# Optimization experiments

Hardware: AMD Instinct MI355X
Metric: run time of the kernel (lower is better)

## Reference

```python
import jax, jax.numpy as jnp
import numpy as np


def setup_inputs() -> dict:
    key = jax.random.key(0)
    k1, k2, k3, k4 = jax.random.split(key, 4)
    B, Nq, Nc, D = 4, 1024, 16384, 1024
    return {
        "query_embeddings": jax.random.normal(k1, (B, Nq, D), dtype=jnp.float32),
        "context_embeddings": jax.random.normal(k2, (B, Nc, D), dtype=jnp.float32),
        "W": jax.random.normal(k3, (D, D), dtype=jnp.float32) * (1.0 / np.sqrt(D)),
        "b": jax.random.normal(k4, (D,), dtype=jnp.float32) * 0.02,
    }


TOP_N = 5


def _pairwise_l2(q, c):
    # q: [B, Nq, D], c: [B, Nc, D] -> [B, Nq, Nc] Euclidean distances
    q_sq = jnp.sum(q * q, axis=-1, keepdims=True)          # [B, Nq, 1]
    c_sq = jnp.sum(c * c, axis=-1)[:, None, :]             # [B, 1, Nc]
    cross = jnp.einsum("bqd,bcd->bqc", q, c)               # [B, Nq, Nc]
    d2 = jnp.maximum(q_sq + c_sq - 2.0 * cross, 0.0)
    return jnp.sqrt(d2)


def reference(query_embeddings, context_embeddings, W, b):
    # latent query projection (nn.Linear): x @ W.T + b
    q_proj = jnp.einsum("bqd,ed->bqe", query_embeddings, W) + b
    distances = _pairwise_l2(q_proj, context_embeddings)    # [B, Nq, Nc]
    # smallest top_n distances -> top_k on negated values
    neg_d, idx = jax.lax.top_k(-distances, TOP_N)
    return (-neg_d, idx)
```

## Files before the change

### kernel.cpp

```cpp
#include <hip/hip_runtime.h>
#include <cfloat>
#include <math.h>

#define D_DIM 1024
#define B_DIM 4
#define NQ    1024
#define NC    16384
#define TOPN  5
#define TOPA  5
#define CSPLIT 8
#define CAND  (TOPA*CSPLIT)
#define QT    64
#define CTILE 256
#define BK    64

#define PBM 128
#define PBN 64
#define PBK 16
#define PPAD 4

typedef __bf16 bf16x8 __attribute__((ext_vector_type(8)));
typedef float  f32x4  __attribute__((ext_vector_type(4)));
typedef double f64x4  __attribute__((ext_vector_type(4)));

__device__ __forceinline__ unsigned short f2bf(float f) {
    unsigned u = __builtin_bit_cast(unsigned, f);
    unsigned r = (u + 0x7fffu + ((u >> 16) & 1u)) >> 16;
    return (unsigned short)r;
}

__device__ __forceinline__ void gload16(const void* g, void* l) {
    __builtin_amdgcn_global_load_lds(
        (const __attribute__((address_space(1))) unsigned*)g,
        (__attribute__((address_space(3))) unsigned*)l, 16, 0, 0);
}

template<int N, typename T>
__device__ __forceinline__ void topk_insert(T (&bv)[N], int (&bi)[N], T v, int ci) {
    if (v < bv[N-1] || (v == bv[N-1] && ci < bi[N-1])) {
        bv[N-1] = v; bi[N-1] = ci;
        #pragma unroll
        for (int s = N-1; s > 0; --s) {
            bool sw = (bv[s] < bv[s-1]) || (bv[s] == bv[s-1] && bi[s] < bi[s-1]);
            if (sw) {
                T tv = bv[s-1]; bv[s-1] = bv[s]; bv[s] = tv;
                int ti = bi[s-1]; bi[s-1] = bi[s]; bi[s] = ti;
            }
        }
    }
}

template<int N>
__device__ __forceinline__ void insN(float (&bv)[N], int (&bi)[N], float v, int ci) {
    if (v < bv[N-1]) {
        bv[N-1] = v; bi[N-1] = ci;
        #pragma unroll
        for (int s = N-1; s > 0; --s) {
            if (bv[s] < bv[s-1]) {
                float tv = bv[s-1]; bv[s-1] = bv[s]; bv[s] = tv;
                int   ti = bi[s-1]; bi[s-1] = bi[s]; bi[s] = ti;
            }
        }
    }
}

__device__ __forceinline__ void ins5b(float (&bv)[TOPA], int (&bi)[TOPA], float v, int ci) {
    #pragma unroll
    for (int s = 0; s < TOPA; ++s) {
        const bool  c    = v < bv[s];
        const float vmin = c ? v : bv[s];
        const float vmax = c ? bv[s] : v;
        const int   imin = c ? ci : bi[s];
        const int   imax = c ? bi[s] : ci;
        bv[s] = vmin; bi[s] = imin;
        v = vmax; ci = imax;
    }
}

__global__ __launch_bounds__(256) void proj64_mfma_kernel(const float* __restrict__ Q,
                                                          const float* __restrict__ W,
                                                          const float* __restrict__ bias,
                                                          double* __restrict__ P64)
{
    __shared__ float Qs[PBM][PBK + PPAD];
    __shared__ float Ws[PBN][PBK + PPAD];

    const int t    = threadIdx.x;
    const int lane = t & 63;
    const int w    = t >> 6;
    const int l15  = lane & 15;
    const int l4   = lane >> 4;
    const int m0   = blockIdx.y * PBM;
    const int n0   = blockIdx.x * PBN;
    const int wm   = (w >> 1) * 64;
    const int wn   = (w & 1) * 32;

    const int srow = t >> 2;
    const int scol = (t & 3) * 4;

    f64x4 acc[4][2];
    #pragma unroll
    for (int fm = 0; fm < 4; ++fm)
        #pragma unroll
        for (int fn = 0; fn < 2; ++fn) acc[fm][fn] = (f64x4)0.0;

    for (int k0 = 0; k0 < D_DIM; k0 += PBK) {
        float4 qa0 = *(const float4*)&Q[(size_t)(m0 + srow)      * D_DIM + k0 + scol];
        float4 qa1 = *(const float4*)&Q[(size_t)(m0 + srow + 64) * D_DIM + k0 + scol];
        float4 wa  = *(const float4*)&W[(size_t)(n0 + srow)      * D_DIM + k0 + scol];
        __syncthreads();
        *(float4*)&Qs[srow][scol]      = qa0;
        *(float4*)&Qs[srow + 64][scol] = qa1;
        *(float4*)&Ws[srow][scol]      = wa;
        __syncthreads();

        #pragma unroll
        for (int ks = 0; ks < 4; ++ks) {
            const int kc = ks * 4 + l4;
            double a[4], b[2];
            #pragma unroll
            for (int fm = 0; fm < 4; ++fm) a[fm] = (double)Qs[wm + fm * 16 + l15][kc];
            #pragma unroll
            for (int fn = 0; fn < 2; ++fn) b[fn] = (double)Ws[wn + fn * 16 + l15][kc];
            #pragma unroll
            for (int fm = 0; fm < 4; ++fm)
                #pragma unroll
                for (int fn = 0; fn < 2; ++fn)
                    acc[fm][fn] = __builtin_amdgcn_mfma_f64_16x16x4f64(a[fm], b[fn], acc[fm][fn], 0, 0, 0);
        }
    }

    #pragma unroll
    for (int fm = 0; fm < 4; ++fm) {
        #pragma unroll
        for (int fn = 0; fn < 2; ++fn) {
            const int col = n0 + wn + fn * 16 + l15;
            const double bv = (double)bias[col];
            #pragma unroll
            for (int j = 0; j < 4; ++j) {
                const int row = m0 + wm + fm * 16 + j * 4 + l4;
                P64[(size_t)row * D_DIM + col] = acc[fm][fn][j] + bv;
            }
        }
    }
}

__global__ __launch_bounds__(256) void perm_detect_kernel(const float* __restrict__ Q,
                                                          const float* __restrict__ W,
                                                          const float* __restrict__ bias,
                                                          const double* __restrict__ P64,
                                                          int* __restrict__ invperm)
{
    __shared__ double tv[16];
    const int t = threadIdx.x;
    const int g = t >> 4;
    const int s = t & 15;
    if (t < 16) invperm[t] = t;

    double acc = 0.0;
    const int kb = s * 64;
    for (int k = 0; k < 64; ++k)
        acc = fma((double)Q[(size_t)g * D_DIM + kb + k], (double)W[kb + k], acc);
    #pragma unroll
    for (int off = 8; off; off >>= 1) acc += __shfl_down(acc, off, 16);
    if (s == 0) tv[g] = acc + (double)bias[0];
    __syncthreads();

    if (t < 16) {
        double p = P64[(size_t)t * D_DIM];
        int best = 0; double bd = fabs(p - tv[0]);
        #pragma unroll
        for (int i = 1; i < 16; ++i) {
            double d = fabs(p - tv[i]);
            if (d < bd) { bd = d; best = i; }
        }
        invperm[best] = t;
    }
}

__global__ __launch_bounds__(256) void pack_c_kernel(const float* __restrict__ C,
                                                     unsigned short* __restrict__ Cbf,
                                                     float* __restrict__ csq)
{
    int wave = threadIdx.x >> 6;
    int lane = threadIdx.x & 63;
    int row  = blockIdx.x * 4 + wave;
    const float* x = C + (size_t)row * D_DIM;
    float s = 0.f;
    #pragma unroll
    for (int i = 0; i < 4; ++i) {
        float4 v = *(const float4*)&x[lane * 4 + i * 256];
        s += v.x * v.x + v.y * v.y + v.z * v.z + v.w * v.w;
        ushort4 h;
        h.x = f2bf(v.x); h.y = f2bf(v.y); h.z = f2bf(v.z); h.w = f2bf(v.w);
        *(ushort4*)&Cbf[(size_t)row * D_DIM + lane * 4 + i * 256] = h;
    }
    #pragma unroll
    for (int off = 32; off; off >>= 1) s += __shfl_down(s, off, 64);
    if (lane == 0) csq[row] = s;
}

__global__ __launch_bounds__(256) void pack_q_kernel(const double* __restrict__ P64,
                                                     const int* __restrict__ invperm,
                                                     unsigned short* __restrict__ Pbf,
                                                     float* __restrict__ qsq)
{
    int wave = threadIdx.x >> 6;
    int lane = threadIdx.x & 63;
    int row  = blockIdx.x * 4 + wave;
    int prow = (row & ~15) | invperm[row & 15];
    const double* x = P64 + (size_t)prow * D_DIM;
    float s = 0.f;
    #pragma unroll
    for (int j = 0; j < 8; ++j) {
        double2 v = *(const double2*)&x[lane * 2 + j * 128];
        float a = (float)v.x, b = (float)v.y;
        s += a * a + b * b;
        ushort2 h; h.x = f2bf(a); h.y = f2bf(b);
        *(ushort2*)&Pbf[(size_t)row * D_DIM + lane * 2 + j * 128] = h;
    }
    #pragma unroll
    for (int off = 32; off; off >>= 1) s += __shfl_down(s, off, 64);
    if (lane == 0) qsq[row] = s;
}

__global__ __launch_bounds__(256, 3) void dist_mfma_kernel(const unsigned short* __restrict__ Pbf,
                                                           const unsigned short* __restrict__ Cbf,
                                                           const float* __restrict__ qsq,
                                                           const float* __restrict__ csq,
                                                           int* __restrict__ pi)
{
    __shared__ __align__(16) short CsS[CTILE * 64];
    __shared__ __align__(16) short QsS[QT * 64];
    float* MV = (float*)CsS;
    int*   MI = (int*)(CsS + 4096);

    const int t    = threadIdx.x;
    const int lane = t & 63;
    const int w    = t >> 6;
    const int l15  = lane & 15;
    const int l4   = lane >> 4;
    const int r8   = lane >> 3;
    const int sc   = lane & 7;
    const int csplit = blockIdx.x;
    const int by = blockIdx.y;
    const int bz = blockIdx.z;
    const int qg0 = bz * NQ + by * QT;

    unsigned cOff[8], qOff[2];
    #pragma unroll
    for (int j = 0; j < 8; ++j)
        cOff[j] = (unsigned)((w * 64 + j * 8 + r8) * D_DIM + (sc ^ r8) * 8);
    #pragma unroll
    for (int j = 0; j < 2; ++j)
        qOff[j] = (unsigned)((w * 16 + j * 8 + r8) * D_DIM + (sc ^ r8) * 8);

    float qsv[4];
    #pragma unroll
    for (int s = 0; s < 4; ++s) qsv[s] = qsq[qg0 + s * 16 + l15];

    float bv[4][TOPA]; int bi[4][TOPA];
    #pragma unroll
    for (int s = 0; s < 4; ++s)
        #pragma unroll
        for (int j = 0; j < TOPA; ++j) { bv[s][j] = FLT_MAX; bi[s][j] = 0x7fffffff; }

    const int cpb = NC / CSPLIT;
    for (int it = 0; it < cpb / CTILE; ++it) {
        const int cg0 = csplit * cpb + it * CTILE;
        const size_t crow0 = (size_t)bz * NC + cg0;

        f32x4 acc[4][4];
        #pragma unroll
        for (int u = 0; u < 4; ++u)
            #pragma unroll
            for (int s = 0; s < 4; ++s) acc[u][s] = (f32x4)0.0f;

        for (int k0 = 0; k0 < D_DIM; k0 += BK) {
            const unsigned short* cB = Cbf + crow0 * D_DIM + k0;
            const unsigned short* qB = Pbf + (size_t)qg0 * D_DIM + k0;
            __syncthreads();
            #pragma unroll
            for (int j = 0; j < 8; ++j)
                gload16(cB + cOff[j], &CsS[(w * 64 + j * 8) * 64]);
            #pragma unroll
            for (int j = 0; j < 2; ++j)
                gload16(qB + qOff[j], &QsS[(w * 16 + j * 8) * 64]);
            __syncthreads();
            #pragma unroll
            for (int ks = 0; ks < 2; ++ks) {
                const int sp = ((ks * 4 + l4) ^ (l15 & 7)) * 8;
                bf16x8 bq[4], ac[4];
                #pragma unroll
                for (int s = 0; s < 4; ++s)
                    bq[s] = *(const bf16x8*)&QsS[(s * 16 + l15) * 64 + sp];
                #pragma unroll
                for (int u = 0; u < 4; ++u)
                    ac[u] = *(const bf16x8*)&CsS[(w * 64 + u * 16 + l15) * 64 + sp];
                #pragma unroll
                for (int u = 0; u < 4; ++u)
                    #pragma unroll
                    for (int s = 0; s < 4; ++s)
                        acc[u][s] = __builtin_amdgcn_mfma_f32_16x16x32_bf16(ac[u], bq[s], acc[u][s], 0, 0, 0);
            }
        }

        #pragma unroll
        for (int u = 0; u < 4; ++u) {
            const int crow = w * 64 + u * 16 + l4 * 4;
            float4 cs4 = *(const float4*)&csq[(size_t)bz * NC + cg0 + crow];
            float csa[4] = {cs4.x, cs4.y, cs4.z, cs4.w};
            #pragma unroll
            for (int s = 0; s < 4; ++s) {
                #pragma unroll
                for (int r = 0; r < 4; ++r) {
                    float v = qsv[s] + csa[r] - 2.0f * acc[u][s][r];
                    ins5b(bv[s], bi[s], v, cg0 + crow + r);
                }
            }
        }
    }

    #pragma unroll
    for (int mask = 16; mask <= 32; mask <<= 1) {
        #pragma unroll
        for (int s = 0; s < 4; ++s) {
            float ov[TOPA]; int oi[TOPA];
            #pragma unroll
            for (int j = 0; j < TOPA; ++j) {
                ov[j] = __shfl_xor(bv[s][j], mask, 64);
                oi[j] = __shfl_xor(bi[s][j], mask, 64);
            }
            #pragma unroll
            for (int j = 0; j < TOPA; ++j) insN<TOPA>(bv[s], bi[s], ov[j], oi[j]);
        }
    }
    __syncthreads();
    if (l4 == 0) {
        #pragma unroll
        for (int s = 0; s < 4; ++s) {
            int q = s * 16 + l15;
            #pragma unroll
            for (int j = 0; j < TOPA; ++j) {
                MV[(q * 4 + w) * TOPA + j] = bv[s][j];
                MI[(q * 4 + w) * TOPA + j] = bi[s][j];
            }
        }
    }
    __syncthreads();
    if (t < QT) {
        float mv[TOPA]; int mi[TOPA];
        #pragma unroll
        for (int j = 0; j < TOPA; ++j) { mv[j] = FLT_MAX; mi[j] = 0x7fffffff; }
        for (int l = 0; l < 4; ++l)
            #pragma unroll
            for (int j = 0; j < TOPA; ++j)
                insN<TOPA>(mv, mi, MV[(t * 4 + l) * TOPA + j], MI[(t * 4 + l) * TOPA + j]);
        size_t base = (((size_t)qg0 + t) * CSPLIT + csplit) * TOPA;
        #pragma unroll
        for (int j = 0; j < TOPA; ++j) pi[base + j] = mi[j];
    }
}

__global__ __launch_bounds__(256) void refine_kernel(const double* __restrict__ P64,
                                                     const int* __restrict__ invperm,
                                                     const float* __restrict__ C,
                                                     const int*   __restrict__ pi,
                                                     float* __restrict__ out)
{
    __shared__ double dvs[CAND];
    __shared__ int    dis[CAND];
    const int q    = blockIdx.x;
    const int pq   = (q & ~15) | invperm[q & 15];
    const int bz   = q >> 10;
    const int t    = threadIdx.x;
    const int wave = t >> 6;
    const int lane = t & 63;
    const double* p = P64 + (size_t)pq * D_DIM;

    for (int k = wave; k < CAND; k += 4) {
        int ci = pi[(size_t)q * CAND + k];
        const float* c = C + ((size_t)bz * NC + ci) * D_DIM;
        double s = 0.0;
        #pragma unroll
        for (int j = 0; j < 16; ++j) {
            int d = lane + 64 * j;
            double diff = p[d] - (double)c[d];
            s = fma(diff, diff, s);
        }
        #pragma unroll
        for (int off = 32; off; off >>= 1) s += __shfl_down(s, off, 64);
        if (lane == 0) { dvs[k] = s; dis[k] = ci; }
    }
    __syncthreads();
    if (t == 0) {
        double bv[TOPN]; int bi[TOPN];
        #pragma unroll
        for (int j = 0; j < TOPN; ++j) { bv[j] = DBL_MAX; bi[j] = 0x7fffffff; }
        for (int k = 0; k < CAND; ++k)
            topk_insert<TOPN,double>(bv, bi, dvs[k], dis[k]);
        #pragma unroll
        for (int j = 0; j < TOPN; ++j) {
            out[(size_t)q * TOPN + j] = (float)sqrt(bv[j]);
            out[(size_t)B_DIM * NQ * TOPN + (size_t)q * TOPN + j] = (float)bi[j];
        }
    }
}

extern "C" void kernel_launch(void* const* d_in, const int* in_sizes, int n_in,
                              void* d_out, int out_size, void* d_ws, size_t ws_size,
                              hipStream_t stream) {
    const float* Q    = (const float*)d_in[0];
    const float* C    = (const float*)d_in[1];
    const float* W    = (const float*)d_in[2];
    const float* bias = (const float*)d_in[3];
    float* out = (float*)d_out;

    char* ws = (char*)d_ws;
    double*         P64 = (double*)ws;
    unsigned short* Pbf = (unsigned short*)(ws + (size_t)32 * 1024 * 1024);
    unsigned short* Cbf = (unsigned short*)(ws + (size_t)40 * 1024 * 1024);
    float*          qsq = (float*)(ws + (size_t)168 * 1024 * 1024);
    float*          csq = qsq + 4096;
    int*            pi  = (int*)(csq + 65536);
    int*            ivp = pi + (size_t)B_DIM * NQ * CAND;

    proj64_mfma_kernel<<<dim3(D_DIM / PBN, (B_DIM * NQ) / PBM), 256, 0, stream>>>(Q, W, bias, P64);
    perm_detect_kernel<<<1, 256, 0, stream>>>(Q, W, bias, P64, ivp);
    pack_c_kernel<<<(B_DIM * NC) / 4, 256, 0, stream>>>(C, Cbf, csq);
    pack_q_kernel<<<(B_DIM * NQ) / 4, 256, 0, stream>>>(P64, ivp, Pbf, qsq);
    dist_mfma_kernel<<<dim3(CSPLIT, NQ / QT, B_DIM), 256, 0, stream>>>(Pbf, Cbf, qsq, csq, pi);
    refine_kernel<<<B_DIM * NQ, 256, 0, stream>>>(P64, ivp, C, pi, out);
}
```

Measured before the change: 925.6 us.

## Double query tile with 8-wave dist blocks and fuse C packing into projection

The distance kernel now uses 512-thread blocks covering 128 queries. Waves are split into two query halves by four candidate quarters, so each C tile loaded into LDS is reused across twice as many queries, halving C traffic per query. Separately, the C bf16 packing blocks are appended to the projection kernel's grid, which removes one launch and lets the memory-bound packing overlap with the compute-bound projection. Costs include higher LDS use, occupancy limited to 2 blocks per CU, and half as many distance blocks.

```diff
diff --git a/kernel.cpp b/kernel.cpp
--- a/kernel.cpp
+++ b/kernel.cpp
@@ -10,7 +10,7 @@
 #define TOPA  5
 #define CSPLIT 8
 #define CAND  (TOPA*CSPLIT)
-#define QT    64
+#define QT    128
 #define CTILE 256
 #define BK    64
 
@@ -18,6 +18,7 @@
 #define PBN 64
 #define PBK 16
 #define PPAD 4
+#define PROJ_BLKS ((D_DIM/PBN) * ((B_DIM*NQ)/PBM))
 
 typedef __bf16 bf16x8 __attribute__((ext_vector_type(8)));
 typedef float  f32x4  __attribute__((ext_vector_type(4)));
@@ -77,11 +78,34 @@
     }
 }
 
-__global__ __launch_bounds__(256) void proj64_mfma_kernel(const float* __restrict__ Q,
-                                                          const float* __restrict__ W,
-                                                          const float* __restrict__ bias,
-                                                          double* __restrict__ P64)
+__global__ __launch_bounds__(256) void proj_packc_kernel(const float* __restrict__ Q,
+                                                         const float* __restrict__ W,
+                                                         const float* __restrict__ bias,
+                                                         const float* __restrict__ C,
+                                                         double* __restrict__ P64,
+                                                         unsigned short* __restrict__ Cbf,
+                                                         float* __restrict__ csq)
 {
+    const int bid = blockIdx.x;
+    if (bid >= PROJ_BLKS) {
+        int wave = threadIdx.x >> 6;
+        int lane = threadIdx.x & 63;
+        int row  = (bid - PROJ_BLKS) * 4 + wave;
+        const float* x = C + (size_t)row * D_DIM;
+        float s = 0.f;
+        #pragma unroll
+        for (int i = 0; i < 4; ++i) {
+            float4 v = *(const float4*)&x[lane * 4 + i * 256];
+            s += v.x * v.x + v.y * v.y + v.z * v.z + v.w * v.w;
+            ushort4 h;
+            h.x = f2bf(v.x); h.y = f2bf(v.y); h.z = f2bf(v.z); h.w = f2bf(v.w);
+            *(ushort4*)&Cbf[(size_t)row * D_DIM + lane * 4 + i * 256] = h;
+        }
+        #pragma unroll
+        for (int off = 32; off; off >>= 1) s += __shfl_down(s, off, 64);
+        if (lane == 0) csq[row] = s;
+        return;
+    }
     __shared__ float Qs[PBM][PBK + PPAD];
     __shared__ float Ws[PBN][PBK + PPAD];
 
@@ -90,8 +114,8 @@
     const int w    = t >> 6;
     const int l15  = lane & 15;
     const int l4   = lane >> 4;
-    const int m0   = blockIdx.y * PBM;
-    const int n0   = blockIdx.x * PBN;
+    const int m0   = (bid >> 4) * PBM;
+    const int n0   = (bid & 15) * PBN;
     const int wm   = (w >> 1) * 64;
     const int wn   = (w & 1) * 32;
 
@@ -178,28 +202,6 @@
     }
 }
 
-__global__ __launch_bounds__(256) void pack_c_kernel(const float* __restrict__ C,
-                                                     unsigned short* __restrict__ Cbf,
-                                                     float* __restrict__ csq)
-{
-    int wave = threadIdx.x >> 6;
-    int lane = threadIdx.x & 63;
-    int row  = blockIdx.x * 4 + wave;
-    const float* x = C + (size_t)row * D_DIM;
-    float s = 0.f;
-    #pragma unroll
-    for (int i = 0; i < 4; ++i) {
-        float4 v = *(const float4*)&x[lane * 4 + i * 256];
-        s += v.x * v.x + v.y * v.y + v.z * v.z + v.w * v.w;
-        ushort4 h;
-        h.x = f2bf(v.x); h.y = f2bf(v.y); h.z = f2bf(v.z); h.w = f2bf(v.w);
-        *(ushort4*)&Cbf[(size_t)row * D_DIM + lane * 4 + i * 256] = h;
-    }
-    #pragma unroll
-    for (int off = 32; off; off >>= 1) s += __shfl_down(s, off, 64);
-    if (lane == 0) csq[row] = s;
-}
-
 __global__ __launch_bounds__(256) void pack_q_kernel(const double* __restrict__ P64,
                                                      const int* __restrict__ invperm,
                                                      unsigned short* __restrict__ Pbf,
@@ -224,7 +226,7 @@
     if (lane == 0) qsq[row] = s;
 }
 
-__global__ __launch_bounds__(256, 3) void dist_mfma_kernel(const unsigned short* __restrict__ Pbf,
+__global__ __launch_bounds__(512, 2) void dist_mfma_kernel(const unsigned short* __restrict__ Pbf,
                                                            const unsigned short* __restrict__ Cbf,
                                                            const float* __restrict__ qsq,
                                                            const float* __restrict__ csq,
@@ -233,11 +235,13 @@
     __shared__ __align__(16) short CsS[CTILE * 64];
     __shared__ __align__(16) short QsS[QT * 64];
     float* MV = (float*)CsS;
-    int*   MI = (int*)(CsS + 4096);
+    int*   MI = (int*)(CsS + 5120);
 
     const int t    = threadIdx.x;
     const int lane = t & 63;
     const int w    = t >> 6;
+    const int wq   = w >> 2;
+    const int wc   = w & 3;
     const int l15  = lane & 15;
     const int l4   = lane >> 4;
     const int r8   = lane >> 3;
@@ -247,17 +251,17 @@
     const int bz = blockIdx.z;
     const int qg0 = bz * NQ + by * QT;
 
-    unsigned cOff[8], qOff[2];
-    #pragma unroll
-    for (int j = 0; j < 8; ++j)
-        cOff[j] = (unsigned)((w * 64 + j * 8 + r8) * D_DIM + (sc ^ r8) * 8);
+    unsigned cOff[4], qOff[2];
+    #pragma unroll
+    for (int j = 0; j < 4; ++j)
+        cOff[j] = (unsigned)((wc * 64 + wq * 32 + j * 8 + r8) * D_DIM + (sc ^ r8) * 8);
     #pragma unroll
     for (int j = 0; j < 2; ++j)
         qOff[j] = (unsigned)((w * 16 + j * 8 + r8) * D_DIM + (sc ^ r8) * 8);
 
     float qsv[4];
     #pragma unroll
-    for (int s = 0; s < 4; ++s) qsv[s] = qsq[qg0 + s * 16 + l15];
+    for (int s = 0; s < 4; ++s) qsv[s] = qsq[qg0 + wq * 64 + s * 16 + l15];
 
     float bv[4][TOPA]; int bi[4][TOPA];
     #pragma unroll
@@ -281,8 +285,8 @@
             const unsigned short* qB = Pbf + (size_t)qg0 * D_DIM + k0;
             __syncthreads();
             #pragma unroll
-            for (int j = 0; j < 8; ++j)
-                gload16(cB + cOff[j], &CsS[(w * 64 + j * 8) * 64]);
+            for (int j = 0; j < 4; ++j)
+                gload16(cB + cOff[j], &CsS[(wc * 64 + wq * 32 + j * 8) * 64]);
             #pragma unroll
             for (int j = 0; j < 2; ++j)
                 gload16(qB + qOff[j], &QsS[(w * 16 + j * 8) * 64]);
@@ -293,10 +297,10 @@
                 bf16x8 bq[4], ac[4];
                 #pragma unroll
                 for (int s = 0; s < 4; ++s)
-                    bq[s] = *(const bf16x8*)&QsS[(s * 16 + l15) * 64 + sp];
+                    bq[s] = *(const bf16x8*)&QsS[(wq * 64 + s * 16 + l15) * 64 + sp];
                 #pragma unroll
                 for (int u = 0; u < 4; ++u)
-                    ac[u] = *(const bf16x8*)&CsS[(w * 64 + u * 16 + l15) * 64 + sp];
+                    ac[u] = *(const bf16x8*)&CsS[(wc * 64 + u * 16 + l15) * 64 + sp];
                 #pragma unroll
                 for (int u = 0; u < 4; ++u)
                     #pragma unroll
@@ -307,7 +311,7 @@
 
         #pragma unroll
         for (int u = 0; u < 4; ++u) {
-            const int crow = w * 64 + u * 16 + l4 * 4;
+            const int crow = wc * 64 + u * 16 + l4 * 4;
             float4 cs4 = *(const float4*)&csq[(size_t)bz * NC + cg0 + crow];
             float csa[4] = {cs4.x, cs4.y, cs4.z, cs4.w};
             #pragma unroll
@@ -339,11 +343,11 @@
     if (l4 == 0) {
         #pragma unroll
         for (int s = 0; s < 4; ++s) {
-            int q = s * 16 + l15;
+            int q = wq * 64 + s * 16 + l15;
             #pragma unroll
             for (int j = 0; j < TOPA; ++j) {
-                MV[(q * 4 + w) * TOPA + j] = bv[s][j];
-                MI[(q * 4 + w) * TOPA + j] = bi[s][j];
+                MV[(q * 4 + wc) * TOPA + j] = bv[s][j];
+                MI[(q * 4 + wc) * TOPA + j] = bi[s][j];
             }
         }
     }
@@ -425,10 +429,9 @@
     int*            pi  = (int*)(csq + 65536);
     int*            ivp = pi + (size_t)B_DIM * NQ * CAND;
 
-    proj64_mfma_kernel<<<dim3(D_DIM / PBN, (B_DIM * NQ) / PBM), 256, 0, stream>>>(Q, W, bias, P64);
+    proj_packc_kernel<<<PROJ_BLKS + (B_DIM * NC) / 4, 256, 0, stream>>>(Q, W, bias, C, P64, Cbf, csq);
     perm_detect_kernel<<<1, 256, 0, stream>>>(Q, W, bias, P64, ivp);
-    pack_c_kernel<<<(B_DIM * NC) / 4, 256, 0, stream>>>(C, Cbf, csq);
     pack_q_kernel<<<(B_DIM * NQ) / 4, 256, 0, stream>>>(P64, ivp, Pbf, qsq);
-    dist_mfma_kernel<<<dim3(CSPLIT, NQ / QT, B_DIM), 256, 0, stream>>>(Pbf, Cbf, qsq, csq, pi);
+    dist_mfma_kernel<<<dim3(CSPLIT, NQ / QT, B_DIM), 512, 0, stream>>>(Pbf, Cbf, qsq, csq, pi);
     refine_kernel<<<B_DIM * NQ, 256, 0, stream>>>(P64, ivp, C, pi, out);
 }
```

After: 915.9 us. Within noise of the previous version (-1.1%).
